# Optimization experiments

Hardware: AMD Instinct MI355X
Metric: run time of the kernel (lower is better)

The kernel has to match this reference:

```python
import jax, jax.numpy as jnp
import numpy as np

TEMP = 0.1   # temperature
EPS = 1e-5   # BatchNorm eps
NEG = -1e9   # mask value for excluded logits

def _conv3x3(x, w):
    return jax.lax.conv_general_dilated(x, w, (1, 1), 'SAME',
                                        dimension_numbers=('NCHW', 'OIHW', 'NCHW'))

def _bn(x, gamma, beta, axes):
    # training-mode BatchNorm2d: stats over `axes` (per-sample (2,3) for the
    # single-sample anchor path, batch (0,2,3) for the dense-key path)
    m = x.mean(axes, keepdims=True)
    v = x.var(axes, keepdims=True)
    return gamma[None, :, None, None] * (x - m) * jax.lax.rsqrt(v + EPS) + beta[None, :, None, None]

def _encode(x, p, axes):
    # GranularityEncoder: conv3x3 -> BN -> ReLU -> conv1x1 -> BN -> ReLU -> GAP
    w1, g1, b1, w2, g2, b2 = p
    h = jax.nn.relu(_bn(_conv3x3(x, w1), g1, b1, axes))
    h = jnp.einsum('nchw,oc->nohw', h, w2)
    h = jax.nn.relu(_bn(h, g2, b2, axes))
    return h.mean((2, 3))  # [N, D]

def _norm(x):
    return x / jnp.maximum(jnp.linalg.norm(x, axis=-1, keepdims=True), 1e-12)

def _loss(sparse, dense, params, decision_mask):
    # Anchors: original encodes one sample at a time -> per-sample BN stats (2,3)
    Q = jnp.stack([_norm(_encode(s, p, (2, 3))) for s, p in zip(sparse, params)])        # [G,cav,D]
    # Dense keys: encoded as a full batch under no_grad -> batch BN stats, stop_gradient
    K = jax.lax.stop_gradient(
        jnp.stack([_norm(_encode(d, p, (0, 2, 3))) for d, p in zip(dense, params)]))     # [G,cav,D]
    S = jnp.einsum('gid,gjd->gij', Q, K)                     # same-granularity sims
    pos = jnp.diagonal(S, axis1=1, axis2=2)                  # [G,cav] l_pos
    cav = S.shape[1]
    S_m = jnp.where(jnp.eye(cav, dtype=bool)[None], NEG, S)  # inter-agent negatives (j != i)
    X = jnp.einsum('gid,hid->gih', Q, K)                     # cross-granularity, same agent
    X_m = jnp.where(jnp.eye(3, dtype=bool)[:, None, :], NEG, X)
    logits = jnp.concatenate([pos[..., None], S_m, X_m], axis=-1) / TEMP  # [G,cav,1+cav+3]
    loss_tab = -logits[..., 0] + jax.nn.logsumexp(logits, axis=-1)        # CE with label 0
    # The per-element loss only depends on (agent, granularity): weight by mask counts.
    cnt = jnp.stack([(decision_mask == g + 1).sum((1, 2)) for g in range(3)]).astype(jnp.float32)  # [G,cav-1]
    cnt = jnp.pad(cnt, ((0, 0), (1, 0)))  # agent 0 is never an anchor (loop starts at i=1)
    tot = cnt.sum()
    return jnp.where(tot > 0, (cnt * loss_tab).sum() / jnp.maximum(tot, 1.0), 0.0)

def setup_inputs():
    key = jax.random.key(0)
    ks = jax.random.split(key, 16)
    CAV, H, W, D = 5, 256, 256, 128
    C = {'g1': 64, 'g2': 32, 'g3': 16}
    inp = {}
    i = 0
    for name, c in C.items():
        inp['sparse_' + name] = jax.random.normal(ks[i], (CAV, c, H, W), jnp.float32); i += 1
        inp['dense_' + name] = jax.random.normal(ks[i], (CAV, c, H, W), jnp.float32); i += 1
        inp['w1_' + name] = jax.random.normal(ks[i], (64, c, 3, 3), jnp.float32) * 0.05; i += 1
        inp['bn1_gamma_' + name] = jnp.ones((64,), jnp.float32)
        inp['bn1_beta_' + name] = jnp.zeros((64,), jnp.float32)
        inp['w2_' + name] = jax.random.normal(ks[i], (D, 64), jnp.float32) * 0.05; i += 1
        inp['bn2_gamma_' + name] = jnp.ones((D,), jnp.float32)
        inp['bn2_beta_' + name] = jnp.zeros((D,), jnp.float32)
    inp['decision_mask'] = jax.random.randint(ks[i], (CAV - 1, 128, 128), 0, 4, jnp.int32)
    return inp

def reference(sparse_g1, dense_g1, w1_g1, bn1_gamma_g1, bn1_beta_g1, w2_g1, bn2_gamma_g1, bn2_beta_g1,
              sparse_g2, dense_g2, w1_g2, bn1_gamma_g2, bn1_beta_g2, w2_g2, bn2_gamma_g2, bn2_beta_g2,
              sparse_g3, dense_g3, w1_g3, bn1_gamma_g3, bn1_beta_g3, w2_g3, bn2_gamma_g3, bn2_beta_g3,
              decision_mask):
    sparse = [sparse_g1, sparse_g2, sparse_g3]
    dense = [dense_g1, dense_g2, dense_g3]
    params = [(w1_g1, bn1_gamma_g1, bn1_beta_g1, w2_g1, bn2_gamma_g1, bn2_beta_g1),
              (w1_g2, bn1_gamma_g2, bn1_beta_g2, w2_g2, bn2_gamma_g2, bn2_beta_g2),
              (w1_g3, bn1_gamma_g3, bn1_beta_g3, w2_g3, bn2_gamma_g3, bn2_beta_g3)]
    return _loss(sparse, dense, params, decision_mask)
```

## Files before the change

### kernel.cpp

```cpp
#include <hip/hip_runtime.h>
#include <math.h>

#define HW 65536
#define NS 5
#define DFEAT 128
#define CMID 64
#define TEMPER 0.1f
#define BNEPS 1e-5f

typedef __attribute__((ext_vector_type(8))) short bf16x8;
typedef __attribute__((ext_vector_type(4))) float f32x4;

__device__ inline short f2bf(float f) {
  union { float f; unsigned u; } v; v.f = f;
  unsigned r = v.u + 0x7fffu + ((v.u >> 16) & 1u);
  return (short)(r >> 16);
}
__device__ inline float bf2f(unsigned short h) {
  union { unsigned u; float f; } v; v.u = ((unsigned)h) << 16;
  return v.f;
}

union U16B { int4 v; unsigned short s[8]; };

__global__ void zero_kernel(float* __restrict__ p, int n) {
  int i = blockIdx.x * blockDim.x + threadIdx.x;
  if (i < n) p[i] = 0.f;
}

template<int C, int CP>
__global__ __launch_bounds__(256) void transpose_kernel(const float* __restrict__ x,
                                                        unsigned short* __restrict__ xT) {
  __shared__ float t[64 * (CP + 1)];
  const int tid = threadIdx.x;
  const int n = blockIdx.y;
  const int pix0 = blockIdx.x * 64;
  const float* xn = x + (size_t)n * C * HW + pix0;
#pragma unroll
  for (int it = 0; it < CP * 64 / 256; ++it) {
    int idx = it * 256 + tid;
    int c = idx >> 6, pix = idx & 63;
    float v = (c < C) ? xn[(size_t)c * HW + pix] : 0.f;
    t[pix * (CP + 1) + c] = v;
  }
  __syncthreads();
  unsigned* out = (unsigned*)(xT + ((size_t)n * HW + pix0) * CP);
#pragma unroll
  for (int it = 0; it < 64 * CP / 2 / 256; ++it) {
    int idx = it * 256 + tid;
    int cp = idx & (CP / 2 - 1), pix = idx / (CP / 2);
    float f0 = t[pix * (CP + 1) + 2 * cp];
    float f1 = t[pix * (CP + 1) + 2 * cp + 1];
    unsigned u = ((unsigned)(unsigned short)f2bf(f0)) |
                 (((unsigned)(unsigned short)f2bf(f1)) << 16);
    out[pix * (CP / 2) + cp] = u;
  }
}

template<int C, int CP>
__global__ void wprep_kernel(const float* __restrict__ w1, const float* __restrict__ w2,
                             unsigned short* __restrict__ w1p, unsigned short* __restrict__ w2p) {
  const int KS = CP / 32;
  const int total1 = 9 * KS * 2 * 64 * 32;
  int idx = blockIdx.x * 256 + threadIdx.x;
  if (idx < total1) {
    int kl = idx & 31; int tmp = idx >> 5;
    int nn = tmp & 63; tmp >>= 6;
    int hl = tmp & 1;  tmp >>= 1;
    int ks = tmp % KS; int s = tmp / KS;
    int ic = ks * 32 + kl;
    float v = (ic < C) ? w1[((size_t)nn * C + ic) * 9 + s] : 0.f;
    short hi = f2bf(v);
    short r = (hl == 0) ? hi : f2bf(v - bf2f((unsigned short)hi));
    w1p[idx] = (unsigned short)r;
  } else if (idx < total1 + 2 * 2 * 128 * 32) {
    int i2 = idx - total1;
    int kl = i2 & 31;
    int nn = (i2 >> 5) & 127;
    int hl = (i2 >> 12) & 1;
    int ks = i2 >> 13;
    float v = w2[nn * 64 + ks * 32 + kl];
    short hi = f2bf(v);
    short r = (hl == 0) ? hi : f2bf(v - bf2f((unsigned short)hi));
    w2p[i2] = (unsigned short)r;
  }
}

template<int CP>
__global__ __launch_bounds__(256, 2) void conv_mfma_kernel(
    const unsigned short* __restrict__ xT,
    const unsigned short* __restrict__ w1p,
    unsigned short* __restrict__ h1,
    float* __restrict__ st)
{
  const int KS = CP / 32;
  constexpr int XSB = 10 * 34 * CP * 2;
  constexpr int HSB = 256 * 72 * 2;
  constexpr int UNI = (XSB > HSB) ? XSB : HSB;
  __shared__ __align__(16) char smem[UNI];
  __shared__ float reds[4][64], redq[4][64];

  const int tid = threadIdx.x;
  const int lane = tid & 63, wave = tid >> 6;
  const int lanen = lane & 15, quad = lane >> 4;
  const int tx = blockIdx.x, ty = blockIdx.y, n = blockIdx.z;
  const int x0 = tx * 32, y0 = ty * 8;

  unsigned short* xs = (unsigned short*)smem;
  const int ROWB = 34 * CP * 2;
  const int xstart = (tx == 0) ? 1 : 0;
  const int xend = (tx == 7) ? 33 : 34;
  for (int r = wave; r < 10; r += 4) {
    int gy = y0 - 1 + r;
    char* rowb = smem + r * ROWB;
    if ((unsigned)gy >= 256u) {
      for (int ofs = lane * 16; ofs < ROWB; ofs += 1024)
        *(int4*)(rowb + ofs) = make_int4(0, 0, 0, 0);
    } else {
      const char* g = (const char*)(xT + ((size_t)n * HW + gy * 256 + x0 - 1 + xstart) * CP);
      int nbytes = (xend - xstart) * CP * 2;
      char* dst = rowb + xstart * CP * 2;
      for (int ofs = lane * 16; ofs < nbytes; ofs += 1024)
        *(int4*)(dst + ofs) = *(const int4*)(g + ofs);
      if (xstart == 1) {
        for (int ofs = lane * 16; ofs < CP * 2; ofs += 1024)
          *(int4*)(rowb + ofs) = make_int4(0, 0, 0, 0);
      }
      if (xend == 33) {
        for (int ofs = lane * 16; ofs < CP * 2; ofs += 1024)
          *(int4*)(rowb + 33 * CP * 2 + ofs) = make_int4(0, 0, 0, 0);
      }
    }
  }
  __syncthreads();

  f32x4 acc[4][4];
#pragma unroll
  for (int t = 0; t < 4; ++t)
#pragma unroll
    for (int nt = 0; nt < 4; ++nt)
      acc[t][nt] = (f32x4){0.f, 0.f, 0.f, 0.f};

  int pbase[4];
#pragma unroll
  for (int t = 0; t < 4; ++t) {
    int p = wave * 64 + t * 16 + lanen;
    pbase[t] = (p >> 5) * 34 + (p & 31);
  }

#pragma unroll
  for (int s = 0; s < 9; ++s) {
    const int dy = s / 3, dx = s % 3;
#pragma unroll
    for (int ks = 0; ks < KS; ++ks) {
      bf16x8 af[4];
#pragma unroll
      for (int t = 0; t < 4; ++t) {
        int eo = (pbase[t] + dy * 34 + dx) * CP + ks * 32 + quad * 8;
        af[t] = *(const bf16x8*)(xs + eo);
      }
#pragma unroll
      for (int hl = 0; hl < 2; ++hl) {
        const unsigned short* wb = w1p + ((((s * KS + ks) * 2 + hl) * 64) + lanen) * 32 + quad * 8;
#pragma unroll
        for (int nt = 0; nt < 4; ++nt) {
          bf16x8 bf = *(const bf16x8*)(wb + nt * 16 * 32);
#pragma unroll
          for (int t = 0; t < 4; ++t)
            acc[t][nt] = __builtin_amdgcn_mfma_f32_16x16x32_bf16(af[t], bf, acc[t][nt], 0, 0, 0);
        }
      }
    }
  }

#pragma unroll
  for (int nt = 0; nt < 4; ++nt) {
    float s = 0.f, q = 0.f;
#pragma unroll
    for (int t = 0; t < 4; ++t)
#pragma unroll
      for (int r = 0; r < 4; ++r) {
        float v = acc[t][nt][r];
        s += v; q += v * v;
      }
    s += __shfl_xor(s, 16); s += __shfl_xor(s, 32);
    q += __shfl_xor(q, 16); q += __shfl_xor(q, 32);
    if (lane < 16) { reds[wave][nt * 16 + lanen] = s; redq[wave][nt * 16 + lanen] = q; }
  }
  __syncthreads();
  if (tid < 64) {
    float s = reds[0][tid] + reds[1][tid] + reds[2][tid] + reds[3][tid];
    float q = redq[0][tid] + redq[1][tid] + redq[2][tid] + redq[3][tid];
    atomicAdd(&st[(n * 64 + tid) * 2 + 0], s);
    atomicAdd(&st[(n * 64 + tid) * 2 + 1], q);
  }

  unsigned short* hs = (unsigned short*)smem;
#pragma unroll
  for (int t = 0; t < 4; ++t)
#pragma unroll
    for (int nt = 0; nt < 4; ++nt)
#pragma unroll
      for (int r = 0; r < 4; ++r) {
        int pix = wave * 64 + t * 16 + quad * 4 + r;
        hs[pix * 72 + nt * 16 + lanen] = (unsigned short)f2bf(acc[t][nt][r]);
      }
  __syncthreads();
#pragma unroll
  for (int it = 0; it < 8; ++it) {
    int idx = it * 256 + tid;
    int ocg = idx & 7, pix = idx >> 3;
    int py = pix >> 5, px = pix & 31;
    int4 v = *(const int4*)(hs + pix * 72 + ocg * 8);
    *(int4*)(h1 + ((size_t)n * HW + (y0 + py) * 256 + x0 + px) * 64 + ocg * 8) = v;
  }
}

__global__ void bn_param_kernel(const float* __restrict__ st,
                                const float* __restrict__ gamma,
                                const float* __restrict__ beta,
                                float* __restrict__ a, float* __restrict__ b,
                                int nch, int batchmode)
{
  int tid = threadIdx.x;
  if (tid >= NS * nch) return;
  int n = tid / nch, ch = tid % nch;
  float s, q, cnt;
  if (batchmode) {
    s = 0.f; q = 0.f;
    for (int m = 0; m < NS; ++m) { s += st[(m * nch + ch) * 2]; q += st[(m * nch + ch) * 2 + 1]; }
    cnt = (float)NS * (float)HW;
  } else {
    s = st[(n * nch + ch) * 2]; q = st[(n * nch + ch) * 2 + 1];
    cnt = (float)HW;
  }
  float mean = s / cnt;
  float var = q / cnt - mean * mean;
  float inv = rsqrtf(var + BNEPS);
  float av = gamma[ch] * inv;
  a[n * nch + ch] = av;
  b[n * nch + ch] = beta[ch] - mean * av;
}

template<bool GAP>
__global__ __launch_bounds__(256, 2) void stage2_mfma_kernel(
    const unsigned short* __restrict__ h1,
    const unsigned short* __restrict__ w2p,
    const float* __restrict__ a1g, const float* __restrict__ b1g,
    const float* __restrict__ a2g, const float* __restrict__ b2g,
    float* __restrict__ out)
{
  __shared__ __align__(16) unsigned short acts[256 * 64];
  __shared__ float red[4][128], redq[4][128];
  const int tid = threadIdx.x;
  const int lane = tid & 63, wave = tid >> 6;
  const int lanen = lane & 15, quad = lane >> 4;
  const int n = blockIdx.y;
  const int pix0 = blockIdx.x * 256;

  const int cg = tid & 7;
  float a1c[8], b1c[8];
#pragma unroll
  for (int j = 0; j < 8; ++j) {
    a1c[j] = a1g[n * 64 + cg * 8 + j];
    b1c[j] = b1g[n * 64 + cg * 8 + j];
  }
  const unsigned short* hb = h1 + ((size_t)n * HW + pix0) * 64;
#pragma unroll
  for (int it = 0; it < 8; ++it) {
    int idx = it * 256 + tid;
    int pix = idx >> 3;
    U16B in, o;
    in.v = *(const int4*)(hb + pix * 64 + cg * 8);
#pragma unroll
    for (int j = 0; j < 8; ++j) {
      float f = bf2f(in.s[j]);
      o.s[j] = (unsigned short)f2bf(fmaxf(a1c[j] * f + b1c[j], 0.f));
    }
    *(int4*)(acts + pix * 64 + cg * 8) = o.v;
  }
  __syncthreads();

  f32x4 acc[4][8];
#pragma unroll
  for (int mt = 0; mt < 4; ++mt)
#pragma unroll
    for (int nt = 0; nt < 8; ++nt)
      acc[mt][nt] = (f32x4){0.f, 0.f, 0.f, 0.f};

#pragma unroll
  for (int ks = 0; ks < 2; ++ks) {
    bf16x8 af[4];
#pragma unroll
    for (int mt = 0; mt < 4; ++mt)
      af[mt] = *(const bf16x8*)(acts + (wave * 64 + mt * 16 + lanen) * 64 + ks * 32 + quad * 8);
#pragma unroll
    for (int hl = 0; hl < 2; ++hl) {
      const unsigned short* wb = w2p + (((ks * 2 + hl) * 128) + lanen) * 32 + quad * 8;
#pragma unroll
      for (int nt = 0; nt < 8; ++nt) {
        bf16x8 bf = *(const bf16x8*)(wb + nt * 16 * 32);
#pragma unroll
        for (int mt = 0; mt < 4; ++mt)
          acc[mt][nt] = __builtin_amdgcn_mfma_f32_16x16x32_bf16(af[mt], bf, acc[mt][nt], 0, 0, 0);
      }
    }
  }

  if constexpr (GAP) {
#pragma unroll
    for (int nt = 0; nt < 8; ++nt) {
      int o = nt * 16 + lanen;
      float a2v = a2g[n * DFEAT + o], b2v = b2g[n * DFEAT + o];
      float s = 0.f;
#pragma unroll
      for (int mt = 0; mt < 4; ++mt)
#pragma unroll
        for (int r = 0; r < 4; ++r)
          s += fmaxf(a2v * acc[mt][nt][r] + b2v, 0.f);
      s += __shfl_xor(s, 16); s += __shfl_xor(s, 32);
      if (lane < 16) red[wave][o] = s;
    }
    __syncthreads();
    if (tid < 128)
      atomicAdd(&out[n * DFEAT + tid], red[0][tid] + red[1][tid] + red[2][tid] + red[3][tid]);
  } else {
#pragma unroll
    for (int nt = 0; nt < 8; ++nt) {
      int o = nt * 16 + lanen;
      float s = 0.f, q = 0.f;
#pragma unroll
      for (int mt = 0; mt < 4; ++mt)
#pragma unroll
        for (int r = 0; r < 4; ++r) {
          float v = acc[mt][nt][r];
          s += v; q += v * v;
        }
      s += __shfl_xor(s, 16); s += __shfl_xor(s, 32);
      q += __shfl_xor(q, 16); q += __shfl_xor(q, 32);
      if (lane < 16) { red[wave][o] = s; redq[wave][o] = q; }
    }
    __syncthreads();
    if (tid < 128) {
      atomicAdd(&out[(n * DFEAT + tid) * 2 + 0], red[0][tid] + red[1][tid] + red[2][tid] + red[3][tid]);
      atomicAdd(&out[(n * DFEAT + tid) * 2 + 1], redq[0][tid] + redq[1][tid] + redq[2][tid] + redq[3][tid]);
    }
  }
}

__global__ void feat_kernel(const float* __restrict__ gap, float* __restrict__ QK) {
  int b = blockIdx.x;
  int e = b / 5, n = b % 5;
  int g = e >> 1, br = e & 1;
  int d = threadIdx.x;
  float v = gap[(e * 5 + n) * DFEAT + d] * (1.0f / (float)HW);
  float q = v * v;
  for (int off = 32; off; off >>= 1) q += __shfl_down(q, off, 64);
  __shared__ float r2[2];
  if ((d & 63) == 0) r2[d >> 6] = q;
  __syncthreads();
  float nrm = sqrtf(r2[0] + r2[1]);
  float inv = 1.0f / fmaxf(nrm, 1e-12f);
  QK[((br * 3 + g) * 5 + n) * DFEAT + d] = v * inv;
}

__global__ __launch_bounds__(256) void loss_kernel(const float* __restrict__ QK,
                                                   const int* __restrict__ dm,
                                                   float* __restrict__ out)
{
  __shared__ float Qs[1920], Ks[1920];
  __shared__ float S[75], X[45], cnt[15], ltab[15];
  const int tid = threadIdx.x;
  for (int i = tid; i < 1920; i += 256) { Qs[i] = QK[i]; Ks[i] = QK[1920 + i]; }
  if (tid < 15) cnt[tid] = 0.f;
  __syncthreads();
  if (tid < 75) {
    int g = tid / 25, i = (tid / 5) % 5, j = tid % 5;
    const float* q = &Qs[(g * 5 + i) * 128];
    const float* k = &Ks[(g * 5 + j) * 128];
    float s = 0.f;
    for (int d = 0; d < 128; ++d) s += q[d] * k[d];
    S[tid] = s;
  } else if (tid < 120) {
    int u = tid - 75;
    int g = u / 15, i = (u % 15) / 3, h = u % 3;
    const float* q = &Qs[(g * 5 + i) * 128];
    const float* k = &Ks[(h * 5 + i) * 128];
    float s = 0.f;
    for (int d = 0; d < 128; ++d) s += q[d] * k[d];
    X[u] = s;
  }
  {
    int a = tid >> 6, l = tid & 63;
    int c0 = 0, c1 = 0, c2 = 0;
    const int* base = dm + a * 16384;
    for (int k = 0; k < 256; ++k) {
      int v = base[k * 64 + l];
      c0 += (v == 1); c1 += (v == 2); c2 += (v == 3);
    }
    atomicAdd(&cnt[0 * 5 + a + 1], (float)c0);
    atomicAdd(&cnt[1 * 5 + a + 1], (float)c1);
    atomicAdd(&cnt[2 * 5 + a + 1], (float)c2);
  }
  __syncthreads();
  if (tid < 15) {
    int g = tid / 5, i = tid % 5;
    const float inv_t = 1.0f / TEMPER;
    float lg[9];
    lg[0] = S[g * 25 + i * 5 + i] * inv_t;
    for (int j = 0; j < 5; ++j) lg[1 + j] = (j == i) ? (-1e9f * inv_t) : S[g * 25 + i * 5 + j] * inv_t;
    for (int h = 0; h < 3; ++h) lg[6 + h] = (h == g) ? (-1e9f * inv_t) : X[g * 15 + i * 3 + h] * inv_t;
    float m = lg[0];
    for (int k = 1; k < 9; ++k) m = fmaxf(m, lg[k]);
    float se = 0.f;
    for (int k = 0; k < 9; ++k) se += expf(lg[k] - m);
    ltab[tid] = -lg[0] + m + logf(se);
  }
  __syncthreads();
  if (tid == 0) {
    float tot = 0.f, acc = 0.f;
    for (int k = 0; k < 15; ++k) { tot += cnt[k]; acc += cnt[k] * ltab[k]; }
    out[0] = (tot > 0.f) ? acc / fmaxf(tot, 1.f) : 0.f;
  }
}

extern "C" void kernel_launch(void* const* d_in, const int* in_sizes, int n_in,
                              void* d_out, int out_size, void* d_ws, size_t ws_size,
                              hipStream_t stream) {
  (void)in_sizes; (void)n_in; (void)out_size; (void)ws_size;

  const float* sp[3]  = {(const float*)d_in[0],  (const float*)d_in[8],  (const float*)d_in[16]};
  const float* dn[3]  = {(const float*)d_in[1],  (const float*)d_in[9],  (const float*)d_in[17]};
  const float* w1[3]  = {(const float*)d_in[2],  (const float*)d_in[10], (const float*)d_in[18]};
  const float* gm1[3] = {(const float*)d_in[3],  (const float*)d_in[11], (const float*)d_in[19]};
  const float* bt1[3] = {(const float*)d_in[4],  (const float*)d_in[12], (const float*)d_in[20]};
  const float* w2[3]  = {(const float*)d_in[5],  (const float*)d_in[13], (const float*)d_in[21]};
  const float* gm2[3] = {(const float*)d_in[6],  (const float*)d_in[14], (const float*)d_in[22]};
  const float* bt2[3] = {(const float*)d_in[7],  (const float*)d_in[15], (const float*)d_in[23]};
  const int*   dm     = (const int*)d_in[24];

  float* ws_f = (float*)d_ws;
  unsigned short* h1u  = (unsigned short*)ws_f;
  unsigned short* xTu  = (unsigned short*)(ws_f + 10485760);
  unsigned short* w1pu = (unsigned short*)(ws_f + 20971520);
  unsigned short* w2pu = (unsigned short*)(ws_f + 20971520 + 36864);
  float* st1 = ws_f + 20971520 + 36864 + 8192;
  float* st2 = st1 + 640;
  float* a1  = st2 + 1280;
  float* b1  = a1 + 320;
  float* a2  = b1 + 320;
  float* b2  = a2 + 640;
  float* gap = b2 + 640;
  float* QK  = gap + 3840;

  zero_kernel<<<15, 256, 0, stream>>>(gap, 3840);

  for (int g = 0; g < 3; ++g) {
    if (g == 0)      wprep_kernel<64, 64><<<(9*2*2*64*32 + 16384 + 255)/256, 256, 0, stream>>>(w1[g], w2[g], w1pu, w2pu);
    else if (g == 1) wprep_kernel<32, 32><<<(9*1*2*64*32 + 16384 + 255)/256, 256, 0, stream>>>(w1[g], w2[g], w1pu, w2pu);
    else             wprep_kernel<16, 32><<<(9*1*2*64*32 + 16384 + 255)/256, 256, 0, stream>>>(w1[g], w2[g], w1pu, w2pu);

    for (int br = 0; br < 2; ++br) {
      const int e = g * 2 + br;
      const float* x = br ? dn[g] : sp[g];

      if (g == 0)      transpose_kernel<64, 64><<<dim3(1024, 5), 256, 0, stream>>>(x, xTu);
      else if (g == 1) transpose_kernel<32, 32><<<dim3(1024, 5), 256, 0, stream>>>(x, xTu);
      else             transpose_kernel<16, 32><<<dim3(1024, 5), 256, 0, stream>>>(x, xTu);

      zero_kernel<<<8, 256, 0, stream>>>(st1, 1920);

      if (g == 0) conv_mfma_kernel<64><<<dim3(8, 32, 5), 256, 0, stream>>>(xTu, w1pu, h1u, st1);
      else        conv_mfma_kernel<32><<<dim3(8, 32, 5), 256, 0, stream>>>(xTu, w1pu, h1u, st1);

      bn_param_kernel<<<1, 320, 0, stream>>>(st1, gm1[g], bt1[g], a1, b1, CMID, br);
      stage2_mfma_kernel<false><<<dim3(256, 5), 256, 0, stream>>>(h1u, w2pu, a1, b1, nullptr, nullptr, st2);
      bn_param_kernel<<<1, 640, 0, stream>>>(st2, gm2[g], bt2[g], a2, b2, DFEAT, br);
      stage2_mfma_kernel<true><<<dim3(256, 5), 256, 0, stream>>>(h1u, w2pu, a1, b1, a2, b2, gap + e * 640);
    }
  }

  feat_kernel<<<30, 128, 0, stream>>>(gap, QK);
  loss_kernel<<<1, 256, 0, stream>>>(QK, dm, (float*)d_out);
}
```

Baseline: 1.309 ms.

## Fuse transpose into conv, inline BN params, swizzle LDS, merge launches

The separate NCHW-to-NHWC bf16 transpose kernel is removed: the conv kernel now reads fp32 input directly, converts it to bf16 and writes it into an XOR-swizzled LDS tile, which removes the xT round trip through global memory. The BN-parameter kernels and feat_kernel are folded into stage2 and loss_kernel, and weight prep for all three granularities runs in a single launch. Stage2 now uses 128-pixel blocks with waves split across output channels, LDS swizzle and higher launch bounds to raise occupancy. The conv loads are less coalesced (strided per-channel float4 reads) and each stage2 block recomputes the BN stats, trading redundant work for fewer launches.

```diff
diff --git a/kernel.cpp b/kernel.cpp
--- a/kernel.cpp
+++ b/kernel.cpp
@@ -20,6 +20,9 @@
   union { unsigned u; float f; } v; v.u = ((unsigned)h) << 16;
   return v.f;
 }
+__device__ inline unsigned pack2bf(float f0, float f1) {
+  return ((unsigned)(unsigned short)f2bf(f0)) | (((unsigned)(unsigned short)f2bf(f1)) << 16);
+}
 
 union U16B { int4 v; unsigned short s[8]; };
 
@@ -28,76 +31,53 @@
   if (i < n) p[i] = 0.f;
 }
 
-template<int C, int CP>
-__global__ __launch_bounds__(256) void transpose_kernel(const float* __restrict__ x,
-                                                        unsigned short* __restrict__ xT) {
-  __shared__ float t[64 * (CP + 1)];
-  const int tid = threadIdx.x;
-  const int n = blockIdx.y;
-  const int pix0 = blockIdx.x * 64;
-  const float* xn = x + (size_t)n * C * HW + pix0;
-#pragma unroll
-  for (int it = 0; it < CP * 64 / 256; ++it) {
-    int idx = it * 256 + tid;
-    int c = idx >> 6, pix = idx & 63;
-    float v = (c < C) ? xn[(size_t)c * HW + pix] : 0.f;
-    t[pix * (CP + 1) + c] = v;
-  }
-  __syncthreads();
-  unsigned* out = (unsigned*)(xT + ((size_t)n * HW + pix0) * CP);
-#pragma unroll
-  for (int it = 0; it < 64 * CP / 2 / 256; ++it) {
-    int idx = it * 256 + tid;
-    int cp = idx & (CP / 2 - 1), pix = idx / (CP / 2);
-    float f0 = t[pix * (CP + 1) + 2 * cp];
-    float f1 = t[pix * (CP + 1) + 2 * cp + 1];
-    unsigned u = ((unsigned)(unsigned short)f2bf(f0)) |
-                 (((unsigned)(unsigned short)f2bf(f1)) << 16);
-    out[pix * (CP / 2) + cp] = u;
-  }
-}
-
-template<int C, int CP>
-__global__ void wprep_kernel(const float* __restrict__ w1, const float* __restrict__ w2,
-                             unsigned short* __restrict__ w1p, unsigned short* __restrict__ w2p) {
-  const int KS = CP / 32;
-  const int total1 = 9 * KS * 2 * 64 * 32;
+__global__ void wprep_all_kernel(const float* __restrict__ w1_0, const float* __restrict__ w1_1,
+                                 const float* __restrict__ w1_2, const float* __restrict__ w2_0,
+                                 const float* __restrict__ w2_1, const float* __restrict__ w2_2,
+                                 unsigned short* __restrict__ wp) {
   int idx = blockIdx.x * 256 + threadIdx.x;
-  if (idx < total1) {
-    int kl = idx & 31; int tmp = idx >> 5;
-    int nn = tmp & 63; tmp >>= 6;
-    int hl = tmp & 1;  tmp >>= 1;
-    int ks = tmp % KS; int s = tmp / KS;
+  if (idx < 147456) {
+    int g, local, KS, C;
+    const float* w1;
+    if (idx < 73728)       { g = 0; local = idx;          KS = 2; C = 64; w1 = w1_0; }
+    else if (idx < 110592) { g = 1; local = idx - 73728;  KS = 1; C = 32; w1 = w1_1; }
+    else                   { g = 2; local = idx - 110592; KS = 1; C = 16; w1 = w1_2; }
+    int kl = local & 31; int t = local >> 5;
+    int nn = t & 63; t >>= 6;
+    int hl = t & 1;  t >>= 1;
+    int ks = t % KS; int s = t / KS;
     int ic = ks * 32 + kl;
     float v = (ic < C) ? w1[((size_t)nn * C + ic) * 9 + s] : 0.f;
     short hi = f2bf(v);
     short r = (hl == 0) ? hi : f2bf(v - bf2f((unsigned short)hi));
-    w1p[idx] = (unsigned short)r;
-  } else if (idx < total1 + 2 * 2 * 128 * 32) {
-    int i2 = idx - total1;
-    int kl = i2 & 31;
-    int nn = (i2 >> 5) & 127;
-    int hl = (i2 >> 12) & 1;
-    int ks = i2 >> 13;
+    wp[idx] = (unsigned short)r;
+  } else if (idx < 196608) {
+    int i2 = idx - 147456;
+    int g = i2 >> 14, j = i2 & 16383;
+    const float* w2 = (g == 0) ? w2_0 : (g == 1) ? w2_1 : w2_2;
+    int kl = j & 31;
+    int nn = (j >> 5) & 127;
+    int hl = (j >> 12) & 1;
+    int ks = j >> 13;
     float v = w2[nn * 64 + ks * 32 + kl];
     short hi = f2bf(v);
     short r = (hl == 0) ? hi : f2bf(v - bf2f((unsigned short)hi));
-    w2p[i2] = (unsigned short)r;
-  }
-}
-
-template<int CP>
-__global__ __launch_bounds__(256, 2) void conv_mfma_kernel(
-    const unsigned short* __restrict__ xT,
+    wp[idx] = (unsigned short)r;
+  }
+}
+
+template<int C, int CP>
+__global__ __launch_bounds__(256, 3) void conv_mfma_kernel(
+    const float* __restrict__ x,
     const unsigned short* __restrict__ w1p,
     unsigned short* __restrict__ h1,
     float* __restrict__ st)
 {
-  const int KS = CP / 32;
-  constexpr int XSB = 10 * 34 * CP * 2;
-  constexpr int HSB = 256 * 72 * 2;
-  constexpr int UNI = (XSB > HSB) ? XSB : HSB;
-  __shared__ __align__(16) char smem[UNI];
+  constexpr int KS = CP / 32;
+  constexpr int XS = 10 * 34 * CP;
+  constexpr int HS = 256 * 72;
+  constexpr int UNI = (XS > HS) ? XS : HS;
+  __shared__ __align__(16) unsigned short smem[UNI];
   __shared__ float reds[4][64], redq[4][64];
 
   const int tid = threadIdx.x;
@@ -106,29 +86,46 @@
   const int tx = blockIdx.x, ty = blockIdx.y, n = blockIdx.z;
   const int x0 = tx * 32, y0 = ty * 8;
 
-  unsigned short* xs = (unsigned short*)smem;
-  const int ROWB = 34 * CP * 2;
-  const int xstart = (tx == 0) ? 1 : 0;
-  const int xend = (tx == 7) ? 33 : 34;
-  for (int r = wave; r < 10; r += 4) {
-    int gy = y0 - 1 + r;
-    char* rowb = smem + r * ROWB;
-    if ((unsigned)gy >= 256u) {
-      for (int ofs = lane * 16; ofs < ROWB; ofs += 1024)
-        *(int4*)(rowb + ofs) = make_int4(0, 0, 0, 0);
-    } else {
-      const char* g = (const char*)(xT + ((size_t)n * HW + gy * 256 + x0 - 1 + xstart) * CP);
-      int nbytes = (xend - xstart) * CP * 2;
-      char* dst = rowb + xstart * CP * 2;
-      for (int ofs = lane * 16; ofs < nbytes; ofs += 1024)
-        *(int4*)(dst + ofs) = *(const int4*)(g + ofs);
-      if (xstart == 1) {
-        for (int ofs = lane * 16; ofs < CP * 2; ofs += 1024)
-          *(int4*)(rowb + ofs) = make_int4(0, 0, 0, 0);
-      }
-      if (xend == 33) {
-        for (int ofs = lane * 16; ofs < CP * 2; ofs += 1024)
-          *(int4*)(rowb + 33 * CP * 2 + ofs) = make_int4(0, 0, 0, 0);
+  {
+    constexpr int HALF = CP / 2;
+    for (int idx = tid; idx < 10 * HALF; idx += 256) {
+      const int cp  = idx % HALF;
+      const int row = idx / HALF;
+      const int c0  = cp * 2;
+      const int gy  = y0 - 1 + row;
+      const int grp = c0 >> 3;
+      const int sub = c0 & 7;
+      const bool rowok = ((unsigned)gy < 256u);
+      const bool k0 = rowok && (c0 < C);
+      const bool k1 = rowok && (c0 + 1 < C);
+      const float* g0 = x + (size_t)(n * C + c0) * HW + gy * 256 + x0;
+      const float* g1 = g0 + HW;
+      unsigned short* base = smem + (row * 34) * CP;
+      const int rp = (CP == 32) ? ((row & 1) << 1) : 0;
+      {
+        float v0 = (k0 && tx > 0) ? g0[-1] : 0.f;
+        float v1 = (k1 && tx > 0) ? g1[-1] : 0.f;
+        int ph = (CP == 64) ? grp : ((grp ^ rp) & 3);
+        *(unsigned*)(base + ph * 8 + sub) = pack2bf(v0, v1);
+      }
+      {
+        float v0 = (k0 && tx < 7) ? g0[32] : 0.f;
+        float v1 = (k1 && tx < 7) ? g1[32] : 0.f;
+        int ph = (CP == 64) ? (grp ^ 1) : ((grp ^ 1 ^ rp) & 3);
+        *(unsigned*)(base + 33 * CP + ph * 8 + sub) = pack2bf(v0, v1);
+      }
+#pragma unroll
+      for (int v4 = 0; v4 < 8; ++v4) {
+        float4 f0 = k0 ? ((const float4*)g0)[v4] : make_float4(0.f, 0.f, 0.f, 0.f);
+        float4 f1 = k1 ? ((const float4*)g1)[v4] : make_float4(0.f, 0.f, 0.f, 0.f);
+        const float* a0 = (const float*)&f0;
+        const float* a1 = (const float*)&f1;
+#pragma unroll
+        for (int k = 0; k < 4; ++k) {
+          int col = 1 + v4 * 4 + k;
+          int ph = (CP == 64) ? (grp ^ (col & 7)) : ((grp ^ (col & 3) ^ rp) & 3);
+          *(unsigned*)(base + col * CP + ph * 8 + sub) = pack2bf(a0[k], a1[k]);
+        }
       }
     }
   }
@@ -141,13 +138,6 @@
     for (int nt = 0; nt < 4; ++nt)
       acc[t][nt] = (f32x4){0.f, 0.f, 0.f, 0.f};
 
-  int pbase[4];
-#pragma unroll
-  for (int t = 0; t < 4; ++t) {
-    int p = wave * 64 + t * 16 + lanen;
-    pbase[t] = (p >> 5) * 34 + (p & 31);
-  }
-
 #pragma unroll
   for (int s = 0; s < 9; ++s) {
     const int dy = s / 3, dx = s % 3;
@@ -156,8 +146,12 @@
       bf16x8 af[4];
 #pragma unroll
       for (int t = 0; t < 4; ++t) {
-        int eo = (pbase[t] + dy * 34 + dx) * CP + ks * 32 + quad * 8;
-        af[t] = *(const bf16x8*)(xs + eo);
+        const int row = wave * 2 + (t >> 1) + dy;
+        const int col = (t & 1) * 16 + lanen + dx;
+        int ph;
+        if (CP == 64) ph = (ks * 4 + quad) ^ (col & 7);
+        else          ph = (quad ^ (col & 3) ^ ((row & 1) << 1)) & 3;
+        af[t] = *(const bf16x8*)(smem + (row * 34 + col) * CP + ph * 8);
       }
 #pragma unroll
       for (int hl = 0; hl < 2; ++hl) {
@@ -195,7 +189,6 @@
     atomicAdd(&st[(n * 64 + tid) * 2 + 1], q);
   }
 
-  unsigned short* hs = (unsigned short*)smem;
 #pragma unroll
   for (int t = 0; t < 4; ++t)
 #pragma unroll
@@ -203,7 +196,7 @@
 #pragma unroll
       for (int r = 0; r < 4; ++r) {
         int pix = wave * 64 + t * 16 + quad * 4 + r;
-        hs[pix * 72 + nt * 16 + lanen] = (unsigned short)f2bf(acc[t][nt][r]);
+        smem[pix * 72 + nt * 16 + lanen] = (unsigned short)f2bf(acc[t][nt][r]);
       }
   __syncthreads();
 #pragma unroll
@@ -211,63 +204,54 @@
     int idx = it * 256 + tid;
     int ocg = idx & 7, pix = idx >> 3;
     int py = pix >> 5, px = pix & 31;
-    int4 v = *(const int4*)(hs + pix * 72 + ocg * 8);
+    int4 v = *(const int4*)(smem + pix * 72 + ocg * 8);
     *(int4*)(h1 + ((size_t)n * HW + (y0 + py) * 256 + x0 + px) * 64 + ocg * 8) = v;
   }
 }
 
-__global__ void bn_param_kernel(const float* __restrict__ st,
-                                const float* __restrict__ gamma,
-                                const float* __restrict__ beta,
-                                float* __restrict__ a, float* __restrict__ b,
-                                int nch, int batchmode)
-{
-  int tid = threadIdx.x;
-  if (tid >= NS * nch) return;
-  int n = tid / nch, ch = tid % nch;
-  float s, q, cnt;
-  if (batchmode) {
-    s = 0.f; q = 0.f;
-    for (int m = 0; m < NS; ++m) { s += st[(m * nch + ch) * 2]; q += st[(m * nch + ch) * 2 + 1]; }
-    cnt = (float)NS * (float)HW;
-  } else {
-    s = st[(n * nch + ch) * 2]; q = st[(n * nch + ch) * 2 + 1];
-    cnt = (float)HW;
-  }
-  float mean = s / cnt;
-  float var = q / cnt - mean * mean;
-  float inv = rsqrtf(var + BNEPS);
-  float av = gamma[ch] * inv;
-  a[n * nch + ch] = av;
-  b[n * nch + ch] = beta[ch] - mean * av;
-}
-
 template<bool GAP>
-__global__ __launch_bounds__(256, 2) void stage2_mfma_kernel(
+__global__ __launch_bounds__(256, 3) void stage2_mfma_kernel(
     const unsigned short* __restrict__ h1,
     const unsigned short* __restrict__ w2p,
-    const float* __restrict__ a1g, const float* __restrict__ b1g,
-    const float* __restrict__ a2g, const float* __restrict__ b2g,
-    float* __restrict__ out)
+    const float* __restrict__ st1,
+    const float* __restrict__ st2,
+    const float* __restrict__ gm1, const float* __restrict__ bt1,
+    const float* __restrict__ gm2, const float* __restrict__ bt2,
+    float* __restrict__ outp,
+    int batchmode)
 {
-  __shared__ __align__(16) unsigned short acts[256 * 64];
-  __shared__ float red[4][128], redq[4][128];
+  __shared__ __align__(16) unsigned short acts[128 * 64];
+  __shared__ float red[4][64], redq[4][64];
   const int tid = threadIdx.x;
   const int lane = tid & 63, wave = tid >> 6;
   const int lanen = lane & 15, quad = lane >> 4;
   const int n = blockIdx.y;
-  const int pix0 = blockIdx.x * 256;
+  const int pix0 = blockIdx.x * 128;
 
   const int cg = tid & 7;
   float a1c[8], b1c[8];
 #pragma unroll
   for (int j = 0; j < 8; ++j) {
-    a1c[j] = a1g[n * 64 + cg * 8 + j];
-    b1c[j] = b1g[n * 64 + cg * 8 + j];
-  }
+    int ch = cg * 8 + j;
+    float s, q, cnt;
+    if (batchmode) {
+      s = 0.f; q = 0.f;
+      for (int m = 0; m < NS; ++m) { s += st1[(m * 64 + ch) * 2]; q += st1[(m * 64 + ch) * 2 + 1]; }
+      cnt = (float)NS * (float)HW;
+    } else {
+      s = st1[(n * 64 + ch) * 2]; q = st1[(n * 64 + ch) * 2 + 1];
+      cnt = (float)HW;
+    }
+    float mean = s / cnt;
+    float var = q / cnt - mean * mean;
+    float iv = rsqrtf(var + BNEPS);
+    a1c[j] = gm1[ch] * iv;
+    b1c[j] = bt1[ch] - mean * a1c[j];
+  }
+
   const unsigned short* hb = h1 + ((size_t)n * HW + pix0) * 64;
 #pragma unroll
-  for (int it = 0; it < 8; ++it) {
+  for (int it = 0; it < 4; ++it) {
     int idx = it * 256 + tid;
     int pix = idx >> 3;
     U16B in, o;
@@ -277,28 +261,34 @@
       float f = bf2f(in.s[j]);
       o.s[j] = (unsigned short)f2bf(fmaxf(a1c[j] * f + b1c[j], 0.f));
     }
-    *(int4*)(acts + pix * 64 + cg * 8) = o.v;
-  }
-  __syncthreads();
-
-  f32x4 acc[4][8];
+    int ph = cg ^ (pix & 7);
+    *(int4*)(acts + pix * 64 + ph * 8) = o.v;
+  }
+  __syncthreads();
+
+  const int pb = (wave & 1) * 64;
+  const int ob = (wave >> 1) * 64;
+  f32x4 acc[4][4];
 #pragma unroll
   for (int mt = 0; mt < 4; ++mt)
 #pragma unroll
-    for (int nt = 0; nt < 8; ++nt)
+    for (int nt = 0; nt < 4; ++nt)
       acc[mt][nt] = (f32x4){0.f, 0.f, 0.f, 0.f};
 
 #pragma unroll
   for (int ks = 0; ks < 2; ++ks) {
     bf16x8 af[4];
 #pragma unroll
-    for (int mt = 0; mt < 4; ++mt)
-      af[mt] = *(const bf16x8*)(acts + (wave * 64 + mt * 16 + lanen) * 64 + ks * 32 + quad * 8);
+    for (int mt = 0; mt < 4; ++mt) {
+      int pix = pb + mt * 16 + lanen;
+      int ph = (ks * 4 + quad) ^ (pix & 7);
+      af[mt] = *(const bf16x8*)(acts + pix * 64 + ph * 8);
+    }
 #pragma unroll
     for (int hl = 0; hl < 2; ++hl) {
-      const unsigned short* wb = w2p + (((ks * 2 + hl) * 128) + lanen) * 32 + quad * 8;
-#pragma unroll
-      for (int nt = 0; nt < 8; ++nt) {
+      const unsigned short* wb = w2p + (((ks * 2 + hl) * 128) + ob + lanen) * 32 + quad * 8;
+#pragma unroll
+      for (int nt = 0; nt < 4; ++nt) {
         bf16x8 bf = *(const bf16x8*)(wb + nt * 16 * 32);
 #pragma unroll
         for (int mt = 0; mt < 4; ++mt)
@@ -309,25 +299,39 @@
 
   if constexpr (GAP) {
 #pragma unroll
-    for (int nt = 0; nt < 8; ++nt) {
-      int o = nt * 16 + lanen;
-      float a2v = a2g[n * DFEAT + o], b2v = b2g[n * DFEAT + o];
+    for (int nt = 0; nt < 4; ++nt) {
+      const int o = ob + nt * 16 + lanen;
+      float s2, q2, cnt2;
+      if (batchmode) {
+        s2 = 0.f; q2 = 0.f;
+        for (int m = 0; m < NS; ++m) { s2 += st2[(m * 128 + o) * 2]; q2 += st2[(m * 128 + o) * 2 + 1]; }
+        cnt2 = (float)NS * (float)HW;
+      } else {
+        s2 = st2[(n * 128 + o) * 2]; q2 = st2[(n * 128 + o) * 2 + 1];
+        cnt2 = (float)HW;
+      }
+      float mean = s2 / cnt2;
+      float var = q2 / cnt2 - mean * mean;
+      float iv = rsqrtf(var + BNEPS);
+      float a2 = gm2[o] * iv;
+      float b2 = bt2[o] - mean * a2;
       float s = 0.f;
 #pragma unroll
       for (int mt = 0; mt < 4; ++mt)
 #pragma unroll
         for (int r = 0; r < 4; ++r)
-          s += fmaxf(a2v * acc[mt][nt][r] + b2v, 0.f);
+          s += fmaxf(a2 * acc[mt][nt][r] + b2, 0.f);
       s += __shfl_xor(s, 16); s += __shfl_xor(s, 32);
-      if (lane < 16) red[wave][o] = s;
+      if (lane < 16) red[wave][nt * 16 + lanen] = s;
     }
     __syncthreads();
-    if (tid < 128)
-      atomicAdd(&out[n * DFEAT + tid], red[0][tid] + red[1][tid] + red[2][tid] + red[3][tid]);
+    if (tid < 128) {
+      int oh = tid >> 6, ol = tid & 63;
+      atomicAdd(&outp[n * DFEAT + tid], red[oh * 2][ol] + red[oh * 2 + 1][ol]);
+    }
   } else {
 #pragma unroll
-    for (int nt = 0; nt < 8; ++nt) {
-      int o = nt * 16 + lanen;
+    for (int nt = 0; nt < 4; ++nt) {
       float s = 0.f, q = 0.f;
 #pragma unroll
       for (int mt = 0; mt < 4; ++mt)
@@ -338,54 +342,47 @@
         }
       s += __shfl_xor(s, 16); s += __shfl_xor(s, 32);
       q += __shfl_xor(q, 16); q += __shfl_xor(q, 32);
-      if (lane < 16) { red[wave][o] = s; redq[wave][o] = q; }
+      if (lane < 16) { red[wave][nt * 16 + lanen] = s; redq[wave][nt * 16 + lanen] = q; }
     }
     __syncthreads();
     if (tid < 128) {
-      atomicAdd(&out[(n * DFEAT + tid) * 2 + 0], red[0][tid] + red[1][tid] + red[2][tid] + red[3][tid]);
-      atomicAdd(&out[(n * DFEAT + tid) * 2 + 1], redq[0][tid] + redq[1][tid] + redq[2][tid] + redq[3][tid]);
-    }
-  }
-}
-
-__global__ void feat_kernel(const float* __restrict__ gap, float* __restrict__ QK) {
-  int b = blockIdx.x;
-  int e = b / 5, n = b % 5;
-  int g = e >> 1, br = e & 1;
-  int d = threadIdx.x;
-  float v = gap[(e * 5 + n) * DFEAT + d] * (1.0f / (float)HW);
-  float q = v * v;
-  for (int off = 32; off; off >>= 1) q += __shfl_down(q, off, 64);
-  __shared__ float r2[2];
-  if ((d & 63) == 0) r2[d >> 6] = q;
-  __syncthreads();
-  float nrm = sqrtf(r2[0] + r2[1]);
-  float inv = 1.0f / fmaxf(nrm, 1e-12f);
-  QK[((br * 3 + g) * 5 + n) * DFEAT + d] = v * inv;
-}
-
-__global__ __launch_bounds__(256) void loss_kernel(const float* __restrict__ QK,
+      int oh = tid >> 6, ol = tid & 63;
+      atomicAdd(&outp[(n * DFEAT + tid) * 2 + 0], red[oh * 2][ol] + red[oh * 2 + 1][ol]);
+      atomicAdd(&outp[(n * DFEAT + tid) * 2 + 1], redq[oh * 2][ol] + redq[oh * 2 + 1][ol]);
+    }
+  }
+}
+
+__global__ __launch_bounds__(256) void loss_kernel(const float* __restrict__ gap,
                                                    const int* __restrict__ dm,
                                                    float* __restrict__ out)
 {
-  __shared__ float Qs[1920], Ks[1920];
-  __shared__ float S[75], X[45], cnt[15], ltab[15];
+  __shared__ float F[3840];
+  __shared__ float S[75], X[45], cnt[15], ltab[15], inv[30];
   const int tid = threadIdx.x;
-  for (int i = tid; i < 1920; i += 256) { Qs[i] = QK[i]; Ks[i] = QK[1920 + i]; }
+  for (int i = tid; i < 3840; i += 256) F[i] = gap[i] * (1.0f / (float)HW);
   if (tid < 15) cnt[tid] = 0.f;
+  __syncthreads();
+  if (tid < 30) {
+    float q = 0.f;
+    for (int d = 0; d < 128; ++d) { float v = F[tid * 128 + d]; q += v * v; }
+    inv[tid] = 1.0f / fmaxf(sqrtf(q), 1e-12f);
+  }
+  __syncthreads();
+  for (int i = tid; i < 3840; i += 256) F[i] *= inv[i >> 7];
   __syncthreads();
   if (tid < 75) {
     int g = tid / 25, i = (tid / 5) % 5, j = tid % 5;
-    const float* q = &Qs[(g * 5 + i) * 128];
-    const float* k = &Ks[(g * 5 + j) * 128];
+    const float* q = &F[(2 * g) * 640 + i * 128];
+    const float* k = &F[(2 * g + 1) * 640 + j * 128];
     float s = 0.f;
     for (int d = 0; d < 128; ++d) s += q[d] * k[d];
     S[tid] = s;
   } else if (tid < 120) {
     int u = tid - 75;
     int g = u / 15, i = (u % 15) / 3, h = u % 3;
-    const float* q = &Qs[(g * 5 + i) * 128];
-    const float* k = &Ks[(h * 5 + i) * 128];
+    const float* q = &F[(2 * g) * 640 + i * 128];
+    const float* k = &F[(2 * h + 1) * 640 + i * 128];
     float s = 0.f;
     for (int d = 0; d < 128; ++d) s += q[d] * k[d];
     X[u] = s;
@@ -440,46 +437,36 @@
   const int*   dm     = (const int*)d_in[24];
 
   float* ws_f = (float*)d_ws;
-  unsigned short* h1u  = (unsigned short*)ws_f;
-  unsigned short* xTu  = (unsigned short*)(ws_f + 10485760);
-  unsigned short* w1pu = (unsigned short*)(ws_f + 20971520);
-  unsigned short* w2pu = (unsigned short*)(ws_f + 20971520 + 36864);
-  float* st1 = ws_f + 20971520 + 36864 + 8192;
-  float* st2 = st1 + 640;
-  float* a1  = st2 + 1280;
-  float* b1  = a1 + 320;
-  float* a2  = b1 + 320;
-  float* b2  = a2 + 640;
-  float* gap = b2 + 640;
-  float* QK  = gap + 3840;
-
-  zero_kernel<<<15, 256, 0, stream>>>(gap, 3840);
+  unsigned short* h1u = (unsigned short*)ws_f;
+  unsigned short* wp  = (unsigned short*)(ws_f + 10485760);
+  float* st1_all = ws_f + 10485760 + 98304;
+  float* st2_all = st1_all + 3840;
+  float* gap     = st2_all + 7680;
+  const int W1OFF[3] = {0, 73728, 110592};
+  const int W2OFF[3] = {147456, 163840, 180224};
+
+  zero_kernel<<<60, 256, 0, stream>>>(st1_all, 15360);
+  wprep_all_kernel<<<768, 256, 0, stream>>>(w1[0], w1[1], w1[2], w2[0], w2[1], w2[2], wp);
 
   for (int g = 0; g < 3; ++g) {
-    if (g == 0)      wprep_kernel<64, 64><<<(9*2*2*64*32 + 16384 + 255)/256, 256, 0, stream>>>(w1[g], w2[g], w1pu, w2pu);
-    else if (g == 1) wprep_kernel<32, 32><<<(9*1*2*64*32 + 16384 + 255)/256, 256, 0, stream>>>(w1[g], w2[g], w1pu, w2pu);
-    else             wprep_kernel<16, 32><<<(9*1*2*64*32 + 16384 + 255)/256, 256, 0, stream>>>(w1[g], w2[g], w1pu, w2pu);
-
     for (int br = 0; br < 2; ++br) {
       const int e = g * 2 + br;
       const float* x = br ? dn[g] : sp[g];
-
-      if (g == 0)      transpose_kernel<64, 64><<<dim3(1024, 5), 256, 0, stream>>>(x, xTu);
-      else if (g == 1) transpose_kernel<32, 32><<<dim3(1024, 5), 256, 0, stream>>>(x, xTu);
-      else             transpose_kernel<16, 32><<<dim3(1024, 5), 256, 0, stream>>>(x, xTu);
-
-      zero_kernel<<<8, 256, 0, stream>>>(st1, 1920);
-
-      if (g == 0) conv_mfma_kernel<64><<<dim3(8, 32, 5), 256, 0, stream>>>(xTu, w1pu, h1u, st1);
-      else        conv_mfma_kernel<32><<<dim3(8, 32, 5), 256, 0, stream>>>(xTu, w1pu, h1u, st1);
-
-      bn_param_kernel<<<1, 320, 0, stream>>>(st1, gm1[g], bt1[g], a1, b1, CMID, br);
-      stage2_mfma_kernel<false><<<dim3(256, 5), 256, 0, stream>>>(h1u, w2pu, a1, b1, nullptr, nullptr, st2);
-      bn_param_kernel<<<1, 640, 0, stream>>>(st2, gm2[g], bt2[g], a2, b2, DFEAT, br);
-      stage2_mfma_kernel<true><<<dim3(256, 5), 256, 0, stream>>>(h1u, w2pu, a1, b1, a2, b2, gap + e * 640);
-    }
-  }
-
-  feat_kernel<<<30, 128, 0, stream>>>(gap, QK);
-  loss_kernel<<<1, 256, 0, stream>>>(QK, dm, (float*)d_out);
-}
+      float* st1 = st1_all + e * 640;
+      float* st2 = st2_all + e * 1280;
+
+      dim3 cg(8, 32, 5);
+      if (g == 0)      conv_mfma_kernel<64, 64><<<cg, 256, 0, stream>>>(x, wp + W1OFF[g], h1u, st1);
+      else if (g == 1) conv_mfma_kernel<32, 32><<<cg, 256, 0, stream>>>(x, wp + W1OFF[g], h1u, st1);
+      else             conv_mfma_kernel<16, 32><<<cg, 256, 0, stream>>>(x, wp + W1OFF[g], h1u, st1);
+
+      dim3 sg(512, 5);
+      stage2_mfma_kernel<false><<<sg, 256, 0, stream>>>(h1u, wp + W2OFF[g], st1, nullptr,
+                                                        gm1[g], bt1[g], gm2[g], bt2[g], st2, br);
+      stage2_mfma_kernel<true><<<sg, 256, 0, stream>>>(h1u, wp + W2OFF[g], st1, st2,
+                                                       gm1[g], bt1[g], gm2[g], bt2[g], gap + e * 640, br);
+    }
+  }
+
+  loss_kernel<<<1, 256, 0, stream>>>(gap, dm, (float*)d_out);
+}
```

Measured after the change: 1.693 ms. 1.29x slower.
